# Kernel tuning notes

Measured on AMD Instinct MI355X. Metric: run time of the kernel, lower is better.

Reference implementation:

```python
import jax, jax.numpy as jnp
import numpy as np

N = 100000      # nodes
E = 1600000     # edges
C_IN = 128
H = 64          # hidden_channels
FC = [128, 64, 32, 16]
G = 64          # graphs in batch
EPS = 1e-5


def _glorot(key, fan_in, fan_out):
    s = 1.0 / np.sqrt(fan_in)
    return jax.random.uniform(key, (fan_in, fan_out), jnp.float32, -s, s)


def setup_inputs() -> dict:
    key = jax.random.key(0)
    ks = jax.random.split(key, 24)
    inp = {
        "x": jax.random.normal(ks[0], (N, C_IN), jnp.float32),
        "edge_index": jax.random.randint(ks[1], (2, E), 0, N, jnp.int32),
        "batch": jnp.sort(jax.random.randint(ks[2], (N,), 0, G, jnp.int32)),
        # GCN layers
        "W1": _glorot(ks[3], C_IN, H), "b1": jnp.zeros((H,), jnp.float32),
        "W2": _glorot(ks[4], H, H),    "b2": jnp.zeros((H,), jnp.float32),
        # BatchNorm affine params
        "gamma1": jnp.ones((H,), jnp.float32), "beta1": jnp.zeros((H,), jnp.float32),
        "gamma2": jnp.ones((H,), jnp.float32), "beta2": jnp.zeros((H,), jnp.float32),
        # MLP stack 64->128->64->32->16->1
        "fW1": _glorot(ks[5], H, FC[0]),     "fb1": jnp.zeros((FC[0],), jnp.float32),
        "fW2": _glorot(ks[6], FC[0], FC[1]), "fb2": jnp.zeros((FC[1],), jnp.float32),
        "fW3": _glorot(ks[7], FC[1], FC[2]), "fb3": jnp.zeros((FC[2],), jnp.float32),
        "fW4": _glorot(ks[8], FC[2], FC[3]), "fb4": jnp.zeros((FC[3],), jnp.float32),
        "oW": _glorot(ks[9], FC[3], 1),      "ob": jnp.zeros((1,), jnp.float32),
    }
    return inp


def gcn_conv(x, W, b, src, dst):
    # x' = D^{-1/2} (A + I) D^{-1/2} X W + b   (PyG GCNConv, add_self_loops=True)
    h = x @ W                                             # [N, H]
    loops = jnp.arange(N, dtype=src.dtype)
    s = jnp.concatenate([src, loops])
    d = jnp.concatenate([dst, loops])
    deg = jax.ops.segment_sum(jnp.ones_like(d, jnp.float32), d, num_segments=N)
    dinv = jax.lax.rsqrt(deg)                             # deg >= 1 (self-loops)
    norm = dinv[s] * dinv[d]                              # [E+N]
    msg = h[s] * norm[:, None]                            # gather + scale
    return jax.ops.segment_sum(msg, d, num_segments=N) + b


def batch_norm(x, gamma, beta):
    mu = jnp.mean(x, axis=0)
    var = jnp.mean((x - mu) ** 2, axis=0)                 # biased, as torch BN
    return (x - mu) * jax.lax.rsqrt(var + EPS) * gamma + beta


def reference(x, edge_index, batch, W1, b1, W2, b2, gamma1, beta1, gamma2, beta2,
              fW1, fb1, fW2, fb2, fW3, fb3, fW4, fb4, oW, ob):
    src, dst = edge_index[0], edge_index[1]
    h = jax.nn.relu(gcn_conv(x, W1, b1, src, dst))
    h = batch_norm(h, gamma1, beta1)                      # dropout = identity (eval)
    h = jax.nn.relu(gcn_conv(h, W2, b2, src, dst))
    h = batch_norm(h, gamma2, beta2)
    # global mean pool over graphs
    sums = jax.ops.segment_sum(h, batch, num_segments=G)
    cnts = jax.ops.segment_sum(jnp.ones((N,), jnp.float32), batch, num_segments=G)
    g = sums / jnp.maximum(cnts, 1.0)[:, None]            # [G, H]
    g = jax.nn.relu(g @ fW1 + fb1)
    g = jax.nn.relu(g @ fW2 + fb2)
    g = jax.nn.relu(g @ fW3 + fb3)
    g = jax.nn.relu(g @ fW4 + fb4)
    return g @ oW + ob                                    # [G, 1]
```

## Files before the change

### kernel.cpp

```cpp
#include <hip/hip_runtime.h>
#include <hip/hip_bf16.h>
#include <hip/hip_fp16.h>

#define NNODES 100000
#define NEDGES 1600000
#define NGRAPH 64
#define NCOPY  32
#define NSLOT  8

#define NPART   8
#define PSIZE   (NNODES / NPART)
#define ECH     2048
#define NSLICE  782
#define CAP     48
#define NGEMM1  1563

__global__ __launch_bounds__(256) void k_fill(const int* __restrict__ ei,
                                              unsigned* __restrict__ cnt,
                                              unsigned* __restrict__ colidx) {
    const int p   = blockIdx.x & (NPART - 1);
    const int plo = p * PSIZE;
    const int phi = plo + PSIZE;
    const int s   = blockIdx.x >> 3;
    const int e0  = s * ECH;
    const int e1  = min(e0 + ECH, NEDGES);
    for (int e = e0 + threadIdx.x * 4; e < e1; e += 1024) {
        int4 d = *reinterpret_cast<const int4*>(&ei[NEDGES + e]);
        if (d.x >= plo && d.x < phi) {
            unsigned q = atomicAdd(&cnt[d.x], 1u);
            if (q < CAP) colidx[(unsigned)d.x * CAP + q] = (unsigned)ei[e + 0];
        }
        if (d.y >= plo && d.y < phi) {
            unsigned q = atomicAdd(&cnt[d.y], 1u);
            if (q < CAP) colidx[(unsigned)d.y * CAP + q] = (unsigned)ei[e + 1];
        }
        if (d.z >= plo && d.z < phi) {
            unsigned q = atomicAdd(&cnt[d.z], 1u);
            if (q < CAP) colidx[(unsigned)d.z * CAP + q] = (unsigned)ei[e + 2];
        }
        if (d.w >= plo && d.w < phi) {
            unsigned q = atomicAdd(&cnt[d.w], 1u);
            if (q < CAP) colidx[(unsigned)d.w * CAP + q] = (unsigned)ei[e + 3];
        }
    }
}

__global__ __launch_bounds__(256) void k_dinv(const unsigned* __restrict__ cnt,
                                              float* __restrict__ dinv) {
    int i = (blockIdx.x * 256 + threadIdx.x) * 4;
    if (i < NNODES) {
        uint4 c = *reinterpret_cast<const uint4*>(&cnt[i]);
        float4 r;
        r.x = rsqrtf((float)(c.x + 1u));
        r.y = rsqrtf((float)(c.y + 1u));
        r.z = rsqrtf((float)(c.z + 1u));
        r.w = rsqrtf((float)(c.w + 1u));
        *reinterpret_cast<float4*>(&dinv[i]) = r;
    }
}

__global__ __launch_bounds__(256) void k_gemm1(const float* __restrict__ A,
                                               const float* __restrict__ W,
                                               const float* __restrict__ rowscale,
                                               __half* __restrict__ hd) {
    __shared__ float wlds[64 * 64];
    __shared__ float alds[64 * 68];
    const int tid = threadIdx.x;
    const int tc = (tid & 15) * 4;
    const int tr = (tid >> 4) * 4;
    const int row0 = blockIdx.x * 64;
    float acc[4][4];
    #pragma unroll
    for (int i = 0; i < 4; ++i)
        #pragma unroll
        for (int j = 0; j < 4; ++j) acc[i][j] = 0.f;

    for (int kc = 0; kc < 2; ++kc) {
        for (int idx2 = tid; idx2 < 64 * 16; idx2 += 256) {
            int r = idx2 >> 4, kk = (idx2 & 15) * 4;
            *reinterpret_cast<float4*>(&wlds[r * 64 + kk]) =
                *reinterpret_cast<const float4*>(&W[(kc * 64 + r) * 64 + kk]);
        }
        for (int idx2 = tid; idx2 < 64 * 16; idx2 += 256) {
            int r = idx2 >> 4, kk = (idx2 & 15) * 4;
            int row = row0 + r;
            float4 v = make_float4(0.f, 0.f, 0.f, 0.f);
            if (row < NNODES) v = *reinterpret_cast<const float4*>(&A[row * 128 + kc * 64 + kk]);
            *reinterpret_cast<float4*>(&alds[r * 68 + kk]) = v;
        }
        __syncthreads();
        #pragma unroll 8
        for (int k = 0; k < 64; ++k) {
            float4 wv = *reinterpret_cast<const float4*>(&wlds[k * 64 + tc]);
            float av[4];
            #pragma unroll
            for (int i = 0; i < 4; ++i) av[i] = alds[(tr + i) * 68 + k];
            #pragma unroll
            for (int i = 0; i < 4; ++i) {
                acc[i][0] = fmaf(av[i], wv.x, acc[i][0]);
                acc[i][1] = fmaf(av[i], wv.y, acc[i][1]);
                acc[i][2] = fmaf(av[i], wv.z, acc[i][2]);
                acc[i][3] = fmaf(av[i], wv.w, acc[i][3]);
            }
        }
        __syncthreads();
    }
    #pragma unroll
    for (int i = 0; i < 4; ++i) {
        int row = row0 + tr + i;
        if (row < NNODES) {
            float f = rowscale[row];
            __half2* p = reinterpret_cast<__half2*>(&hd[(size_t)row * 64 + tc]);
            p[0] = __floats2half2_rn(acc[i][0] * f, acc[i][1] * f);
            p[1] = __floats2half2_rn(acc[i][2] * f, acc[i][3] * f);
        }
    }
}

__device__ __forceinline__ void acc_row(const __half* __restrict__ hd, unsigned s, int c0, float4& acc) {
    uint2 u = *reinterpret_cast<const uint2*>(&hd[(size_t)s * 64 + c0]);
    __half2 x01 = *reinterpret_cast<__half2*>(&u.x);
    __half2 x23 = *reinterpret_cast<__half2*>(&u.y);
    float2 f01 = __half22float2(x01);
    float2 f23 = __half22float2(x23);
    acc.x += f01.x; acc.y += f01.y; acc.z += f23.x; acc.w += f23.y;
}

#define WAVE_REDUCE_8(s0,s1,s2,s3,q0,q1,q2,q3)                      \
    {                                                                \
        _Pragma("unroll")                                            \
        for (int m = 16; m < 64; m <<= 1) {                          \
            s0 += __shfl_xor(s0, m); s1 += __shfl_xor(s1, m);        \
            s2 += __shfl_xor(s2, m); s3 += __shfl_xor(s3, m);        \
            q0 += __shfl_xor(q0, m); q1 += __shfl_xor(q1, m);        \
            q2 += __shfl_xor(q2, m); q3 += __shfl_xor(q3, m);        \
        }                                                            \
    }

__global__ __launch_bounds__(256) void k_gather_fused(const unsigned* __restrict__ cnt,
                                                      const unsigned* __restrict__ colidx,
                                                      const __half* __restrict__ hd,
                                                      const float* __restrict__ dinv,
                                                      const float* __restrict__ bias,
                                                      float* __restrict__ act,
                                                      float* bn_sum, float* bn_sq, int n) {
    const int tid = threadIdx.x;
    const int grp = tid >> 4;
    const int c0  = (tid & 15) * 4;
    float4 bv = *reinterpret_cast<const float4*>(&bias[c0]);
    float s0=0.f,s1=0.f,s2=0.f,s3=0.f, q0=0.f,q1=0.f,q2=0.f,q3=0.f;

    #pragma unroll
    for (int it = 0; it < 2; ++it) {
        int node = blockIdx.x * 32 + grp * 2 + it;
        if (node < n) {
            unsigned deg = cnt[node];
            unsigned lo = (unsigned)node * CAP;
            unsigned hi = lo + deg;
            float4 acc = make_float4(0.f, 0.f, 0.f, 0.f);
            acc_row(hd, (unsigned)node, c0, acc);
            unsigned j = lo;
            for (; j + 4 <= hi; j += 4) {
                uint4 a = *reinterpret_cast<const uint4*>(&colidx[j]);
                acc_row(hd, a.x, c0, acc);
                acc_row(hd, a.y, c0, acc);
                acc_row(hd, a.z, c0, acc);
                acc_row(hd, a.w, c0, acc);
            }
            for (; j < hi; ++j) acc_row(hd, colidx[j], c0, acc);
            float w = dinv[node];
            float4 r;
            r.x = fmaxf(fmaf(acc.x, w, bv.x), 0.f);
            r.y = fmaxf(fmaf(acc.y, w, bv.y), 0.f);
            r.z = fmaxf(fmaf(acc.z, w, bv.z), 0.f);
            r.w = fmaxf(fmaf(acc.w, w, bv.w), 0.f);
            *reinterpret_cast<float4*>(&act[(size_t)node * 64 + c0]) = r;
            s0 += r.x; s1 += r.y; s2 += r.z; s3 += r.w;
            q0 = fmaf(r.x, r.x, q0); q1 = fmaf(r.y, r.y, q1);
            q2 = fmaf(r.z, r.z, q2); q3 = fmaf(r.w, r.w, q3);
        }
    }

    WAVE_REDUCE_8(s0,s1,s2,s3,q0,q1,q2,q3);
    __shared__ float ls[4 * 64];
    __shared__ float lq[4 * 64];
    int lane = tid & 63, wid = tid >> 6;
    if (lane < 16) {
        *reinterpret_cast<float4*>(&ls[wid * 64 + lane * 4]) = make_float4(s0, s1, s2, s3);
        *reinterpret_cast<float4*>(&lq[wid * 64 + lane * 4]) = make_float4(q0, q1, q2, q3);
    }
    __syncthreads();
    if (tid < 64) {
        int cpy = (blockIdx.x & (NCOPY - 1)) * 64;
        float S = ls[tid] + ls[64 + tid] + ls[128 + tid] + ls[192 + tid];
        float Q = lq[tid] + lq[64 + tid] + lq[128 + tid] + lq[192 + tid];
        atomicAdd(&bn_sum[cpy + tid], S);
        atomicAdd(&bn_sq[cpy + tid],  Q);
    }
}

__global__ __launch_bounds__(256) void k_gather_pool(const unsigned* __restrict__ cnt,
                                                     const unsigned* __restrict__ colidx,
                                                     const __half* __restrict__ hd,
                                                     const float* __restrict__ dinv,
                                                     const float* __restrict__ bias,
                                                     const int* __restrict__ batch,
                                                     float* __restrict__ gsum,
                                                     float* bn_sum, float* bn_sq, int n) {
    const int tid = threadIdx.x;
    const int grp = tid >> 4;
    const int c0  = (tid & 15) * 4;
    float4 bv = *reinterpret_cast<const float4*>(&bias[c0]);
    float s0=0.f,s1=0.f,s2=0.f,s3=0.f, q0=0.f,q1=0.f,q2=0.f,q3=0.f;

    __shared__ float lds_pool[NSLOT * 64];
    for (int i = tid; i < NSLOT * 64; i += 256) lds_pool[i] = 0.f;
    int node0 = blockIdx.x * 32;
    int g0 = batch[node0 < n ? node0 : (n - 1)];
    __syncthreads();

    #pragma unroll
    for (int it = 0; it < 2; ++it) {
        int node = node0 + grp * 2 + it;
        if (node < n) {
            unsigned deg = cnt[node];
            unsigned lo = (unsigned)node * CAP;
            unsigned hi = lo + deg;
            float4 acc = make_float4(0.f, 0.f, 0.f, 0.f);
            acc_row(hd, (unsigned)node, c0, acc);
            unsigned j = lo;
            for (; j + 4 <= hi; j += 4) {
                uint4 a = *reinterpret_cast<const uint4*>(&colidx[j]);
                acc_row(hd, a.x, c0, acc);
                acc_row(hd, a.y, c0, acc);
                acc_row(hd, a.z, c0, acc);
                acc_row(hd, a.w, c0, acc);
            }
            for (; j < hi; ++j) acc_row(hd, colidx[j], c0, acc);
            float w = dinv[node];
            float4 r;
            r.x = fmaxf(fmaf(acc.x, w, bv.x), 0.f);
            r.y = fmaxf(fmaf(acc.y, w, bv.y), 0.f);
            r.z = fmaxf(fmaf(acc.z, w, bv.z), 0.f);
            r.w = fmaxf(fmaf(acc.w, w, bv.w), 0.f);
            s0 += r.x; s1 += r.y; s2 += r.z; s3 += r.w;
            q0 = fmaf(r.x, r.x, q0); q1 = fmaf(r.y, r.y, q1);
            q2 = fmaf(r.z, r.z, q2); q3 = fmaf(r.w, r.w, q3);
            int slot = batch[node] - g0;
            if (slot < NSLOT) {
                atomicAdd(&lds_pool[slot * 64 + c0 + 0], r.x);
                atomicAdd(&lds_pool[slot * 64 + c0 + 1], r.y);
                atomicAdd(&lds_pool[slot * 64 + c0 + 2], r.z);
                atomicAdd(&lds_pool[slot * 64 + c0 + 3], r.w);
            } else {
                int g = g0 + slot;
                atomicAdd(&gsum[g * 64 + c0 + 0], r.x);
                atomicAdd(&gsum[g * 64 + c0 + 1], r.y);
                atomicAdd(&gsum[g * 64 + c0 + 2], r.z);
                atomicAdd(&gsum[g * 64 + c0 + 3], r.w);
            }
        }
    }

    WAVE_REDUCE_8(s0,s1,s2,s3,q0,q1,q2,q3);
    __shared__ float ls[4 * 64];
    __shared__ float lq[4 * 64];
    int lane = tid & 63, wid = tid >> 6;
    if (lane < 16) {
        *reinterpret_cast<float4*>(&ls[wid * 64 + lane * 4]) = make_float4(s0, s1, s2, s3);
        *reinterpret_cast<float4*>(&lq[wid * 64 + lane * 4]) = make_float4(q0, q1, q2, q3);
    }
    __syncthreads();
    if (tid < 64) {
        int cpy = (blockIdx.x & (NCOPY - 1)) * 64;
        float S = ls[tid] + ls[64 + tid] + ls[128 + tid] + ls[192 + tid];
        float Q = lq[tid] + lq[64 + tid] + lq[128 + tid] + lq[192 + tid];
        atomicAdd(&bn_sum[cpy + tid], S);
        atomicAdd(&bn_sq[cpy + tid],  Q);
        #pragma unroll
        for (int sl = 0; sl < NSLOT; ++sl) {
            int g = g0 + sl;
            if (g < NGRAPH) {
                float v = lds_pool[sl * 64 + tid];
                if (v != 0.f) atomicAdd(&gsum[g * 64 + tid], v);
            }
        }
    }
}

__global__ void k_bn_fold_w2(const float* __restrict__ bn_sum, const float* __restrict__ bn_sq,
                             const float* __restrict__ gamma, const float* __restrict__ beta,
                             const float* __restrict__ W2, float* __restrict__ W2eff,
                             float* __restrict__ c2, int n) {
    __shared__ float sc[64], sh[64];
    int t = threadIdx.x;
    float S = 0.f, Q = 0.f;
    #pragma unroll
    for (int cpy = 0; cpy < NCOPY; ++cpy) { S += bn_sum[cpy * 64 + t]; Q += bn_sq[cpy * 64 + t]; }
    float inv_n = 1.0f / (float)n;
    float mu  = S * inv_n;
    float var = Q * inv_n - mu * mu;
    float s = gamma[t] * rsqrtf(var + 1e-5f);
    sc[t] = s; sh[t] = beta[t] - mu * s;
    __syncthreads();
    float acc = 0.f;
    for (int k = 0; k < 64; ++k) {
        float w = W2[k * 64 + t];
        W2eff[k * 64 + t] = sc[k] * w;
        acc = fmaf(sh[k], w, acc);
    }
    c2[t] = acc;
}

__global__ __launch_bounds__(256) void k_gemm64_h(const float* __restrict__ A,
                                                  const float* __restrict__ W,
                                                  const float* __restrict__ addvec,
                                                  const float* __restrict__ rowscale,
                                                  __half* __restrict__ hd, int n) {
    __shared__ float wlds[64 * 64];
    __shared__ float alds[64 * 68];
    const int tid = threadIdx.x;
    const int tc  = (tid & 15) * 4;
    const int tr  = (tid >> 4) * 4;
    const int row0 = blockIdx.x * 64;

    float acc[4][4];
    float4 cv = *reinterpret_cast<const float4*>(&addvec[tc]);
    #pragma unroll
    for (int i = 0; i < 4; ++i) { acc[i][0]=cv.x; acc[i][1]=cv.y; acc[i][2]=cv.z; acc[i][3]=cv.w; }

    {
        for (int idx = tid; idx < 64 * 16; idx += 256) {
            int r = idx >> 4, kk = (idx & 15) * 4;
            *reinterpret_cast<float4*>(&wlds[r * 64 + kk]) =
                *reinterpret_cast<const float4*>(&W[r * 64 + kk]);
        }
        for (int idx = tid; idx < 64 * 16; idx += 256) {
            int r = idx >> 4, kk = (idx & 15) * 4;
            int row = row0 + r;
            float4 v = make_float4(0.f, 0.f, 0.f, 0.f);
            if (row < n) v = *reinterpret_cast<const float4*>(&A[row * 64 + kk]);
            *reinterpret_cast<float4*>(&alds[r * 68 + kk]) = v;
        }
        __syncthreads();
        #pragma unroll 8
        for (int k = 0; k < 64; ++k) {
            float4 wv = *reinterpret_cast<const float4*>(&wlds[k * 64 + tc]);
            float av[4];
            #pragma unroll
            for (int i = 0; i < 4; ++i) av[i] = alds[(tr + i) * 68 + k];
            #pragma unroll
            for (int i = 0; i < 4; ++i) {
                acc[i][0] = fmaf(av[i], wv.x, acc[i][0]);
                acc[i][1] = fmaf(av[i], wv.y, acc[i][1]);
                acc[i][2] = fmaf(av[i], wv.z, acc[i][2]);
                acc[i][3] = fmaf(av[i], wv.w, acc[i][3]);
            }
        }
    }
    #pragma unroll
    for (int i = 0; i < 4; ++i) {
        int row = row0 + tr + i;
        if (row < n) {
            float f = rowscale[row];
            __half2* p = reinterpret_cast<__half2*>(&hd[(size_t)row * 64 + tc]);
            p[0] = __floats2half2_rn(acc[i][0] * f, acc[i][1] * f);
            p[1] = __floats2half2_rn(acc[i][2] * f, acc[i][3] * f);
        }
    }
}

__device__ __forceinline__ int lower_bound_i(const int* a, int n, int v) {
    int lo = 0, hi = n;
    while (lo < hi) { int m = (lo + hi) >> 1; if (a[m] < v) lo = m + 1; else hi = m; }
    return lo;
}
__global__ __launch_bounds__(128) void k_mlp(const float* __restrict__ gsum,
                                             const int* __restrict__ batch, int n,
                                             const float* __restrict__ bn_sum, const float* __restrict__ bn_sq,
                                             const float* __restrict__ gamma, const float* __restrict__ beta,
                                             const float* __restrict__ fW1, const float* __restrict__ fb1,
                                             const float* __restrict__ fW2, const float* __restrict__ fb2,
                                             const float* __restrict__ fW3, const float* __restrict__ fb3,
                                             const float* __restrict__ fW4, const float* __restrict__ fb4,
                                             const float* __restrict__ oW,  const float* __restrict__ ob,
                                             float* __restrict__ out) {
    int g = blockIdx.x;
    int t = threadIdx.x;
    __shared__ float a[128], bbuf[128];
    if (t < 64) {
        float S = 0.f, Q = 0.f;
        #pragma unroll
        for (int cpy = 0; cpy < NCOPY; ++cpy) { S += bn_sum[cpy * 64 + t]; Q += bn_sq[cpy * 64 + t]; }
        float inv_n = 1.0f / (float)n;
        float mu  = S * inv_n;
        float var = Q * inv_n - mu * mu;
        float s   = gamma[t] * rsqrtf(var + 1e-5f);
        float sh  = beta[t] - mu * s;
        int lo = lower_bound_i(batch, n, g);
        int hi = lower_bound_i(batch, n, g + 1);
        int cnt = hi - lo;
        a[t] = (cnt > 0) ? (gsum[g * 64 + t] / (float)cnt) * s + sh : 0.f;
    }
    __syncthreads();
    {
        float acc = fb1[t];
        for (int k = 0; k < 64; ++k) acc = fmaf(a[k], fW1[k * 128 + t], acc);
        bbuf[t] = fmaxf(acc, 0.f);
    }
    __syncthreads();
    if (t < 64) {
        float acc = fb2[t];
        for (int k = 0; k < 128; ++k) acc = fmaf(bbuf[k], fW2[k * 64 + t], acc);
        a[t] = fmaxf(acc, 0.f);
    }
    __syncthreads();
    if (t < 32) {
        float acc = fb3[t];
        for (int k = 0; k < 64; ++k) acc = fmaf(a[k], fW3[k * 32 + t], acc);
        bbuf[t] = fmaxf(acc, 0.f);
    }
    __syncthreads();
    if (t < 16) {
        float acc = fb4[t];
        for (int k = 0; k < 32; ++k) acc = fmaf(bbuf[k], fW4[k * 16 + t], acc);
        a[t] = fmaxf(acc, 0.f);
    }
    __syncthreads();
    if (t == 0) {
        float acc = ob[0];
        for (int k = 0; k < 16; ++k) acc = fmaf(a[k], oW[k], acc);
        out[g] = acc;
    }
}

extern "C" void kernel_launch(void* const* d_in, const int* in_sizes, int n_in,
                              void* d_out, int out_size, void* d_ws, size_t ws_size,
                              hipStream_t stream) {
    const float* x      = (const float*)d_in[0];
    const int*   ei     = (const int*)  d_in[1];
    const int*   batch  = (const int*)  d_in[2];
    const float* W1     = (const float*)d_in[3];
    const float* b1     = (const float*)d_in[4];
    const float* W2     = (const float*)d_in[5];
    const float* b2     = (const float*)d_in[6];
    const float* gamma1 = (const float*)d_in[7];
    const float* beta1  = (const float*)d_in[8];
    const float* gamma2 = (const float*)d_in[9];
    const float* beta2  = (const float*)d_in[10];
    const float* fW1    = (const float*)d_in[11];
    const float* fb1    = (const float*)d_in[12];
    const float* fW2    = (const float*)d_in[13];
    const float* fb2    = (const float*)d_in[14];
    const float* fW3    = (const float*)d_in[15];
    const float* fb3    = (const float*)d_in[16];
    const float* fW4    = (const float*)d_in[17];
    const float* fb4    = (const float*)d_in[18];
    const float* oW     = (const float*)d_in[19];
    const float* ob     = (const float*)d_in[20];
    float* out = (float*)d_out;

    const int N = NNODES, G = NGRAPH;

    char* base = (char*)d_ws;
    __half*   hd     = (__half*)base;
    float*    act    = (float*)(base + (size_t)N * 64 * 2);
    unsigned* cnt    = (unsigned*)((char*)act + (size_t)N * 64 * 4);
    float*    dinv   = (float*)(cnt + N);
    unsigned* colidx = (unsigned*)(dinv + N);
    float*    bn1s   = (float*)(colidx + (size_t)N * CAP);
    float*    bn1q   = bn1s + NCOPY * 64;
    float*    bn2s   = bn1q + NCOPY * 64;
    float*    bn2q   = bn2s + NCOPY * 64;
    float*    gsum   = bn2q + NCOPY * 64;
    float*    W2eff  = gsum + (size_t)G * 64;
    float*    c2     = W2eff + 4096;

    hipMemsetAsync(cnt, 0, (size_t)N * 4, stream);
    hipMemsetAsync(bn1s, 0, (size_t)(4 * NCOPY * 64 + G * 64) * sizeof(float), stream);

    k_fill<<<NSLICE * NPART, 256, 0, stream>>>(ei, cnt, colidx);

    k_dinv<<<(N / 4 + 255) / 256, 256, 0, stream>>>(cnt, dinv);

    k_gemm1<<<NGEMM1, 256, 0, stream>>>(x, W1, dinv, hd);

    k_gather_fused<<<(N + 31) / 32, 256, 0, stream>>>(cnt, colidx, hd, dinv, b1, act, bn1s, bn1q, N);
    k_bn_fold_w2<<<1, 64, 0, stream>>>(bn1s, bn1q, gamma1, beta1, W2, W2eff, c2, N);

    k_gemm64_h<<<(N + 63) / 64, 256, 0, stream>>>(act, W2eff, c2, dinv, hd, N);
    k_gather_pool<<<(N + 31) / 32, 256, 0, stream>>>(cnt, colidx, hd, dinv, b2, batch, gsum, bn2s, bn2q, N);

    k_mlp<<<G, 128, 0, stream>>>(gsum, batch, N, bn2s, bn2q, gamma2, beta2,
                                 fW1, fb1, fW2, fb2, fW3, fb3, fW4, fb4, oW, ob, out);
}
```

Baseline: 347.5 us.

## Split edge bucketing into local partition sort and per-partition scatter

The single fill kernel, where each of eight partition blocks re-read every edge chunk's destinations, becomes two passes. The first pass reads each 2048-edge chunk once, bins edges by destination partition through shared-memory atomics, and writes packed (local dst, src) words plus per-partition offsets to a staging buffer that reuses the activation workspace. The second pass has each partition block walk only its own edges from four slices and do the global count atomics and colidx writes. This cuts the redundant edge reads that grew with the partition count, at the cost of an extra launch and a staging write and read.

```diff
diff --git a/kernel.cpp b/kernel.cpp
--- a/kernel.cpp
+++ b/kernel.cpp
@@ -14,33 +14,108 @@
 #define NSLICE  782
 #define CAP     48
 #define NGEMM1  1563
-
-__global__ __launch_bounds__(256) void k_fill(const int* __restrict__ ei,
-                                              unsigned* __restrict__ cnt,
-                                              unsigned* __restrict__ colidx) {
+#define SLB     4
+#define NGRP    196
+
+__global__ __launch_bounds__(256) void k_fill_p1(const int* __restrict__ ei,
+                                                 unsigned* __restrict__ gstage,
+                                                 unsigned* __restrict__ gbase,
+                                                 unsigned* __restrict__ gcntp) {
+    const int s   = blockIdx.x;
+    const int tid = threadIdx.x;
+    const int e0  = s * ECH;
+    const int e1  = min(e0 + ECH, NEDGES);
+
+    __shared__ unsigned lcnt[NPART];
+    __shared__ unsigned basep[NPART];
+    __shared__ __align__(16) unsigned stage[ECH];
+
+    if (tid < NPART) lcnt[tid] = 0u;
+    __syncthreads();
+
+    unsigned vals[8]; unsigned pp[8]; unsigned oo[8]; bool valid[2];
+
+    #pragma unroll
+    for (int h = 0; h < 2; ++h) {
+        int e = e0 + h * 1024 + tid * 4;
+        valid[h] = (e < e1);
+        if (valid[h]) {
+            int4 sv = *reinterpret_cast<const int4*>(&ei[e]);
+            int4 dv = *reinterpret_cast<const int4*>(&ei[NEDGES + e]);
+            {
+                unsigned d = (unsigned)dv.x, p = d / (unsigned)PSIZE, r = d - p * PSIZE;
+                vals[h*4+0] = (r << 17) | (unsigned)sv.x; pp[h*4+0] = p;
+                oo[h*4+0] = atomicAdd(&lcnt[p], 1u);
+            }
+            {
+                unsigned d = (unsigned)dv.y, p = d / (unsigned)PSIZE, r = d - p * PSIZE;
+                vals[h*4+1] = (r << 17) | (unsigned)sv.y; pp[h*4+1] = p;
+                oo[h*4+1] = atomicAdd(&lcnt[p], 1u);
+            }
+            {
+                unsigned d = (unsigned)dv.z, p = d / (unsigned)PSIZE, r = d - p * PSIZE;
+                vals[h*4+2] = (r << 17) | (unsigned)sv.z; pp[h*4+2] = p;
+                oo[h*4+2] = atomicAdd(&lcnt[p], 1u);
+            }
+            {
+                unsigned d = (unsigned)dv.w, p = d / (unsigned)PSIZE, r = d - p * PSIZE;
+                vals[h*4+3] = (r << 17) | (unsigned)sv.w; pp[h*4+3] = p;
+                oo[h*4+3] = atomicAdd(&lcnt[p], 1u);
+            }
+        }
+    }
+    __syncthreads();
+
+    if (tid == 0) {
+        unsigned run = 0;
+        #pragma unroll
+        for (int p = 0; p < NPART; ++p) {
+            basep[p] = run;
+            gbase[s * NPART + p] = run;
+            gcntp[s * NPART + p] = lcnt[p];
+            run += lcnt[p];
+        }
+    }
+    __syncthreads();
+
+    #pragma unroll
+    for (int h = 0; h < 2; ++h) {
+        if (valid[h]) {
+            #pragma unroll
+            for (int j = 0; j < 4; ++j)
+                stage[basep[pp[h*4+j]] + oo[h*4+j]] = vals[h*4+j];
+        }
+    }
+    __syncthreads();
+
+    #pragma unroll
+    for (int idx = 0; idx < 2; ++idx) {
+        int i = tid * 4 + idx * 1024;
+        *reinterpret_cast<uint4*>(&gstage[(size_t)s * ECH + i]) =
+            *reinterpret_cast<const uint4*>(&stage[i]);
+    }
+}
+
+__global__ __launch_bounds__(256) void k_fill_p2(const unsigned* __restrict__ gstage,
+                                                 const unsigned* __restrict__ gbase,
+                                                 const unsigned* __restrict__ gcntp,
+                                                 unsigned* __restrict__ cnt,
+                                                 unsigned* __restrict__ colidx) {
     const int p   = blockIdx.x & (NPART - 1);
     const int plo = p * PSIZE;
-    const int phi = plo + PSIZE;
-    const int s   = blockIdx.x >> 3;
-    const int e0  = s * ECH;
-    const int e1  = min(e0 + ECH, NEDGES);
-    for (int e = e0 + threadIdx.x * 4; e < e1; e += 1024) {
-        int4 d = *reinterpret_cast<const int4*>(&ei[NEDGES + e]);
-        if (d.x >= plo && d.x < phi) {
-            unsigned q = atomicAdd(&cnt[d.x], 1u);
-            if (q < CAP) colidx[(unsigned)d.x * CAP + q] = (unsigned)ei[e + 0];
-        }
-        if (d.y >= plo && d.y < phi) {
-            unsigned q = atomicAdd(&cnt[d.y], 1u);
-            if (q < CAP) colidx[(unsigned)d.y * CAP + q] = (unsigned)ei[e + 1];
-        }
-        if (d.z >= plo && d.z < phi) {
-            unsigned q = atomicAdd(&cnt[d.z], 1u);
-            if (q < CAP) colidx[(unsigned)d.z * CAP + q] = (unsigned)ei[e + 2];
-        }
-        if (d.w >= plo && d.w < phi) {
-            unsigned q = atomicAdd(&cnt[d.w], 1u);
-            if (q < CAP) colidx[(unsigned)d.w * CAP + q] = (unsigned)ei[e + 3];
+    const int g   = blockIdx.x >> 3;
+    const int s0  = g * SLB;
+    const int s1  = min(s0 + SLB, NSLICE);
+    for (int s = s0; s < s1; ++s) {
+        unsigned base = gbase[s * NPART + p];
+        unsigned num  = gcntp[s * NPART + p];
+        const unsigned* q = &gstage[(size_t)s * ECH + base];
+        for (unsigned i = threadIdx.x; i < num; i += 256) {
+            unsigned v   = q[i];
+            unsigned dst = (unsigned)plo + (v >> 17);
+            unsigned src = v & 0x1FFFFu;
+            unsigned slot = atomicAdd(&cnt[dst], 1u);
+            if (slot < CAP) colidx[dst * CAP + slot] = src;
         }
     }
 }
@@ -475,11 +550,15 @@
     float*    gsum   = bn2q + NCOPY * 64;
     float*    W2eff  = gsum + (size_t)G * 64;
     float*    c2     = W2eff + 4096;
+    unsigned* gbase  = (unsigned*)(c2 + 64);
+    unsigned* gcntp  = gbase + NSLICE * NPART;
+    unsigned* gstage = (unsigned*)act;
 
     hipMemsetAsync(cnt, 0, (size_t)N * 4, stream);
     hipMemsetAsync(bn1s, 0, (size_t)(4 * NCOPY * 64 + G * 64) * sizeof(float), stream);
 
-    k_fill<<<NSLICE * NPART, 256, 0, stream>>>(ei, cnt, colidx);
+    k_fill_p1<<<NSLICE, 256, 0, stream>>>(ei, gstage, gbase, gcntp);
+    k_fill_p2<<<NGRP * NPART, 256, 0, stream>>>(gstage, gbase, gcntp, cnt, colidx);
 
     k_dinv<<<(N / 4 + 255) / 256, 256, 0, stream>>>(cnt, dinv);
 
```

Measured after the change: 352.7 us. About the same (+1.5%).

## Build CSR via two-pass partition bucketing with LDS-local atomics

Applied to the files above, without the earlier changes.

Replaces the partitioned global-atomic edge fill, which re-read the edge list once per partition, with a two-pass approach. The first pass reads each edge once, packs the local destination and source into one word, and scatters them into 512-node partition buckets using LDS counters plus one global atomic per bucket per block. The second pass builds each partition's adjacency using LDS atomics and also writes counts and dinv, so the separate dinv kernel goes away. It reuses the activation buffer as staging and relies on a fixed per-bucket capacity (9216) and 17-bit source indices, so edges beyond that capacity are silently dropped.

```diff
diff --git a/kernel.cpp b/kernel.cpp
--- a/kernel.cpp
+++ b/kernel.cpp
@@ -8,54 +8,79 @@
 #define NCOPY  32
 #define NSLOT  8
 
-#define NPART   8
-#define PSIZE   (NNODES / NPART)
-#define ECH     2048
-#define NSLICE  782
 #define CAP     48
 #define NGEMM1  1563
 
-__global__ __launch_bounds__(256) void k_fill(const int* __restrict__ ei,
-                                              unsigned* __restrict__ cnt,
-                                              unsigned* __restrict__ colidx) {
-    const int p   = blockIdx.x & (NPART - 1);
-    const int plo = p * PSIZE;
-    const int phi = plo + PSIZE;
-    const int s   = blockIdx.x >> 3;
-    const int e0  = s * ECH;
-    const int e1  = min(e0 + ECH, NEDGES);
-    for (int e = e0 + threadIdx.x * 4; e < e1; e += 1024) {
-        int4 d = *reinterpret_cast<const int4*>(&ei[NEDGES + e]);
-        if (d.x >= plo && d.x < phi) {
-            unsigned q = atomicAdd(&cnt[d.x], 1u);
-            if (q < CAP) colidx[(unsigned)d.x * CAP + q] = (unsigned)ei[e + 0];
-        }
-        if (d.y >= plo && d.y < phi) {
-            unsigned q = atomicAdd(&cnt[d.y], 1u);
-            if (q < CAP) colidx[(unsigned)d.y * CAP + q] = (unsigned)ei[e + 1];
-        }
-        if (d.z >= plo && d.z < phi) {
-            unsigned q = atomicAdd(&cnt[d.z], 1u);
-            if (q < CAP) colidx[(unsigned)d.z * CAP + q] = (unsigned)ei[e + 2];
-        }
-        if (d.w >= plo && d.w < phi) {
-            unsigned q = atomicAdd(&cnt[d.w], 1u);
-            if (q < CAP) colidx[(unsigned)d.w * CAP + q] = (unsigned)ei[e + 3];
-        }
-    }
-}
-
-__global__ __launch_bounds__(256) void k_dinv(const unsigned* __restrict__ cnt,
-                                              float* __restrict__ dinv) {
-    int i = (blockIdx.x * 256 + threadIdx.x) * 4;
-    if (i < NNODES) {
-        uint4 c = *reinterpret_cast<const uint4*>(&cnt[i]);
-        float4 r;
-        r.x = rsqrtf((float)(c.x + 1u));
-        r.y = rsqrtf((float)(c.y + 1u));
-        r.z = rsqrtf((float)(c.z + 1u));
-        r.w = rsqrtf((float)(c.w + 1u));
-        *reinterpret_cast<float4*>(&dinv[i]) = r;
+#define PSH     9
+#define PSZ2    512
+#define NP2     196
+#define PCAP    9216
+#define EPB     4096
+#define NBP1    391
+
+__global__ __launch_bounds__(1024) void k_bucket(const int* __restrict__ ei,
+                                                 unsigned* __restrict__ pstage,
+                                                 unsigned* __restrict__ pcur) {
+    const int tid = threadIdx.x;
+    __shared__ unsigned lcnt[NP2];
+    __shared__ unsigned lbase[NP2];
+    if (tid < NP2) lcnt[tid] = 0u;
+    __syncthreads();
+
+    int e = blockIdx.x * EPB + tid * 4;
+    bool valid = (e < NEDGES);
+    unsigned v0=0,v1=0,v2=0,v3=0, p0=0,p1=0,p2=0,p3=0, o0=0,o1=0,o2=0,o3=0;
+    if (valid) {
+        int4 sv = *reinterpret_cast<const int4*>(&ei[e]);
+        int4 dv = *reinterpret_cast<const int4*>(&ei[NEDGES + e]);
+        unsigned d;
+        d = (unsigned)dv.x; p0 = d >> PSH; v0 = ((d & (PSZ2-1u)) << 17) | (unsigned)sv.x; o0 = atomicAdd(&lcnt[p0], 1u);
+        d = (unsigned)dv.y; p1 = d >> PSH; v1 = ((d & (PSZ2-1u)) << 17) | (unsigned)sv.y; o1 = atomicAdd(&lcnt[p1], 1u);
+        d = (unsigned)dv.z; p2 = d >> PSH; v2 = ((d & (PSZ2-1u)) << 17) | (unsigned)sv.z; o2 = atomicAdd(&lcnt[p2], 1u);
+        d = (unsigned)dv.w; p3 = d >> PSH; v3 = ((d & (PSZ2-1u)) << 17) | (unsigned)sv.w; o3 = atomicAdd(&lcnt[p3], 1u);
+    }
+    __syncthreads();
+    if (tid < NP2) {
+        unsigned c = lcnt[tid];
+        lbase[tid] = c ? atomicAdd(&pcur[tid], c) : 0u;
+    }
+    __syncthreads();
+    if (valid) {
+        unsigned i0 = lbase[p0] + o0; if (i0 < PCAP) pstage[(size_t)p0 * PCAP + i0] = v0;
+        unsigned i1 = lbase[p1] + o1; if (i1 < PCAP) pstage[(size_t)p1 * PCAP + i1] = v1;
+        unsigned i2 = lbase[p2] + o2; if (i2 < PCAP) pstage[(size_t)p2 * PCAP + i2] = v2;
+        unsigned i3 = lbase[p3] + o3; if (i3 < PCAP) pstage[(size_t)p3 * PCAP + i3] = v3;
+    }
+}
+
+__global__ __launch_bounds__(1024) void k_build(const unsigned* __restrict__ pstage,
+                                                const unsigned* __restrict__ pcur,
+                                                unsigned* __restrict__ cnt,
+                                                float* __restrict__ dinv,
+                                                unsigned* __restrict__ colidx) {
+    const int p   = blockIdx.x;
+    const int tid = threadIdx.x;
+    __shared__ unsigned cl[PSZ2];
+    if (tid < PSZ2) cl[tid] = 0u;
+    __syncthreads();
+    unsigned nedge = min(pcur[p], (unsigned)PCAP);
+    const unsigned* q = &pstage[(size_t)p * PCAP];
+    for (unsigned i = tid; i < nedge; i += 1024) {
+        unsigned v    = q[i];
+        unsigned r    = v >> 17;
+        unsigned src  = v & 0x1FFFFu;
+        unsigned slot = atomicAdd(&cl[r], 1u);
+        unsigned node = ((unsigned)p << PSH) + r;
+        if (slot < CAP) colidx[node * CAP + slot] = src;
+    }
+    __syncthreads();
+    if (tid < PSZ2) {
+        unsigned node = ((unsigned)p << PSH) + (unsigned)tid;
+        if (node < NNODES) {
+            unsigned c = cl[tid];
+            cnt[node]  = c;
+            dinv[node] = rsqrtf((float)(c + 1u));
+        }
     }
 }
 
@@ -475,13 +500,14 @@
     float*    gsum   = bn2q + NCOPY * 64;
     float*    W2eff  = gsum + (size_t)G * 64;
     float*    c2     = W2eff + 4096;
-
-    hipMemsetAsync(cnt, 0, (size_t)N * 4, stream);
+    unsigned* pcur   = (unsigned*)(c2 + 64);
+    unsigned* pstage = (unsigned*)act;
+
+    hipMemsetAsync(pcur, 0, (size_t)NP2 * 4, stream);
     hipMemsetAsync(bn1s, 0, (size_t)(4 * NCOPY * 64 + G * 64) * sizeof(float), stream);
 
-    k_fill<<<NSLICE * NPART, 256, 0, stream>>>(ei, cnt, colidx);
-
-    k_dinv<<<(N / 4 + 255) / 256, 256, 0, stream>>>(cnt, dinv);
+    k_bucket<<<NBP1, 1024, 0, stream>>>(ei, pstage, pcur);
+    k_build<<<NP2, 1024, 0, stream>>>(pstage, pcur, cnt, dinv, colidx);
 
     k_gemm1<<<NGEMM1, 256, 0, stream>>>(x, W1, dinv, hd);
 
```

Measured after the change: 309.2 us. 1.12x faster.
